# Kernel optimization log

Hardware: AMD Instinct MI355X
Metric: run time of the kernel (lower is better)

## Reference

```python
import jax, jax.numpy as jnp
import numpy as np

BATCH = 64
SEQ = 128
EMBED_DIM = 512
H = 1024
VOCAB = 32000


def setup_inputs() -> dict:
    key = jax.random.key(0)
    ks = jax.random.split(key, 10)
    prob = jax.random.randint(ks[0], (BATCH, SEQ), 0, VOCAB, dtype=jnp.int64)
    ans = jax.random.randint(ks[1], (BATCH,), 0, 10, dtype=jnp.int64)
    # nn.Embedding default init: N(0,1)
    embed_table = jax.random.normal(ks[2], (VOCAB, EMBED_DIM), jnp.float32)
    # nn.LSTMCell default init: U(-1/sqrt(h), 1/sqrt(h)), gates packed [i,f,g,o]
    k = 1.0 / np.sqrt(H).astype(np.float32)
    w_ih = jax.random.uniform(ks[3], (4 * H, EMBED_DIM), jnp.float32, -k, k)
    w_hh = jax.random.uniform(ks[4], (4 * H, H), jnp.float32, -k, k)
    b_ih = jax.random.uniform(ks[5], (4 * H,), jnp.float32, -k, k)
    b_hh = jax.random.uniform(ks[6], (4 * H,), jnp.float32, -k, k)
    # ansProj: Linear(h, 1)
    w_ans = jax.random.uniform(ks[7], (1, H), jnp.float32, -k, k)
    b_ans = jax.random.uniform(ks[7], (1,), jnp.float32, -k, k)
    # forward draws 0.01*randn initial states; pass them in for determinism
    h0 = 0.01 * jax.random.normal(ks[8], (BATCH, H), jnp.float32)
    c0 = 0.01 * jax.random.normal(ks[9], (BATCH, H), jnp.float32)
    return dict(prob=prob, ans=ans, embed_table=embed_table, w_ih=w_ih,
                w_hh=w_hh, b_ih=b_ih, b_hh=b_hh, w_ans=w_ans, b_ans=b_ans,
                h0=h0, c0=c0)


def reference(prob, ans, embed_table, w_ih, w_hh, b_ih, b_hh, w_ans, b_ans, h0, c0):
    del ans  # unpacked but unused in the original forward
    batch, seq = prob.shape
    num_unary = (seq - 2) // 2
    emb = embed_table[prob]                        # [B, S, E]
    xs = jnp.swapaxes(emb[:, :seq - 1], 0, 1)      # [T=S-1, B, E]

    def step(carry, x):
        h, c = carry
        gates = x @ w_ih.T + b_ih + h @ w_hh.T + b_hh   # [B, 4H]
        i, f, g, o = jnp.split(gates, 4, axis=-1)
        i = jax.nn.sigmoid(i)
        f = jax.nn.sigmoid(f)
        g = jnp.tanh(g)
        o = jax.nn.sigmoid(o)
        c = f * c + i * g
        h = o * jnp.tanh(c)
        return (h, c), h

    _, hs = jax.lax.scan(step, (h0, c0), xs)       # [T, B, H]
    preds = hs @ w_ans.T + b_ans                   # [T, B, 1]
    sel = preds[num_unary + 2:, :, 0]              # kept steps i > numUnary+1
    return sel.T                                   # [B, T-numUnary-2]
```

## Files before the change

kernel.cpp:

```cpp
#include <hip/hip_runtime.h>
#include <math.h>

#define BATCH   64
#define SEQLEN  128
#define EMBED   512
#define HID     1024
#define NSTEP   127
#define OUT0    65
#define NOUT    62

typedef unsigned short ushort_t;
typedef __attribute__((ext_vector_type(8))) __bf16 bf16x8;
typedef __attribute__((ext_vector_type(4))) float  f32x4;

__device__ __forceinline__ float sigmoidf_(float x) { return 1.f / (1.f + expf(-x)); }

__device__ __forceinline__ ushort_t f2bf(float f) {
    unsigned u = __builtin_bit_cast(unsigned, f);
    unsigned r = (u + 0x7FFFu + ((u >> 16) & 1u)) >> 16;
    return (ushort_t)r;
}
__device__ __forceinline__ float bf2f(ushort_t s) {
    unsigned u = ((unsigned)s) << 16;
    return __builtin_bit_cast(float, u);
}


__global__ __launch_bounds__(256) void init_mfma(
    const float* __restrict__ h0, const float* __restrict__ c0,
    float* __restrict__ cT, ushort_t* __restrict__ hf_hi, ushort_t* __restrict__ hf_lo)
{
    int id = blockIdx.x * 256 + threadIdx.x;
    int u = id >> 6, b = id & 63;
    cT[id] = c0[b * HID + u];
    float h = h0[b * HID + u];
    ushort_t hs = f2bf(h);
    ushort_t ls = f2bf(h - bf2f(hs));
    size_t idx = (((size_t)(u >> 5)) * 4 + (b >> 4)) * 512
               + ((((u & 31) >> 3) * 16) + (b & 15)) * 8 + (u & 7);
    hf_hi[idx] = hs;
    hf_lo[idx] = ls;
}

__global__ __launch_bounds__(256) void embed_frag(
    const int* __restrict__ prob, const float* __restrict__ embed,
    ushort_t* __restrict__ xf_hi, ushort_t* __restrict__ xf_lo)
{
    int t = blockIdx.x;
    for (int e = threadIdx.x; e < 4096; e += 256) {
        int b  = e >> 6;
        int kb = e & 63;
        int k  = kb * 8;
        int tok = prob[b * SEQLEN + t];
        const float* row = embed + (size_t)tok * EMBED + k;
        float4 f0 = *(const float4*)(row);
        float4 f1 = *(const float4*)(row + 4);
        float fv[8] = { f0.x, f0.y, f0.z, f0.w, f1.x, f1.y, f1.z, f1.w };
        bf16x8 hv, lv;
        #pragma unroll
        for (int i = 0; i < 8; ++i) {
            ushort_t hs = f2bf(fv[i]);
            ushort_t ls = f2bf(fv[i] - bf2f(hs));
            hv[i] = __builtin_bit_cast(__bf16, hs);
            lv[i] = __builtin_bit_cast(__bf16, ls);
        }
        size_t idx = (((size_t)t * 16 + (kb >> 2)) * 4 + (b >> 4)) * 512
                   + (((kb & 3) * 16) + (b & 15)) * 8;
        *(bf16x8*)(xf_hi + idx) = hv;
        *(bf16x8*)(xf_lo + idx) = lv;
    }
}

__global__ __launch_bounds__(1024) void lstm_mfma(
    const ushort_t* __restrict__ xf_hi, const ushort_t* __restrict__ xf_lo,
    ushort_t* __restrict__ hf_hi, ushort_t* __restrict__ hf_lo,
    const float* __restrict__ cT,
    const float* __restrict__ w_ih, const float* __restrict__ w_hh,
    const float* __restrict__ b_ih, const float* __restrict__ b_hh,
    const float* __restrict__ w_ans, float* __restrict__ pout,
    int* __restrict__ bar)
{
    extern __shared__ ushort_t smem[];
    ushort_t* a_hi = smem;
    ushort_t* a_lo = smem + 48 * 512;
    float*    redA = (float*)(smem + 96 * 512);
    float*    redB = redA + 2048;

    const int tid = threadIdx.x;
    const int bid = blockIdx.x;
    const int w   = tid >> 6;
    const int wn  = w & 3;
    const int kq  = w >> 2;
    const int L   = tid & 63;
    const int n   = L & 15;
    const int q   = L >> 4;
    const int u0  = bid * 4;
    const int ug  = u0 + q;
    const int bg  = wn * 16 + n;

    int* cnt  = bar + (bid & 7) * 32;
    int* scnt = bar + 256;
    int* go   = bar + 288;

    for (int m = 0; m < 16; ++m) {
        int unit = m >> 2, gate = m & 3;
        size_t rowg = (size_t)gate * HID + u0 + unit;
        for (int k = tid; k < 1536; k += 1024) {
            float f = (k < EMBED) ? w_ih[rowg * EMBED + k]
                                  : w_hh[rowg * HID + (k - EMBED)];
            ushort_t hs = f2bf(f);
            ushort_t ls = f2bf(f - bf2f(hs));
            int off = (k >> 5) * 512 + (((k & 31) >> 3) * 16 + m) * 8 + (k & 7);
            a_hi[off] = hs;
            a_lo[off] = ls;
        }
    }

    float c = cT[ug * 64 + bg];
    float bs[4];
    #pragma unroll
    for (int j = 0; j < 4; ++j) bs[j] = b_ih[j * HID + ug] + b_hh[j * HID + ug];
    const float wansu = w_ans[ug];
    __syncthreads();

    for (int t = 0; t < NSTEP; ++t) {
        f32x4 acc = {0.f, 0.f, 0.f, 0.f};

        {
            const ushort_t* xh = xf_hi + (((size_t)t * 16 + kq * 4) * 4 + wn) * 512 + L * 8;
            const ushort_t* xl = xf_lo + (((size_t)t * 16 + kq * 4) * 4 + wn) * 512 + L * 8;
            bf16x8 bh = *(const bf16x8*)(xh);
            bf16x8 bl = *(const bf16x8*)(xl);
            #pragma unroll
            for (int ks = 0; ks < 4; ++ks) {
                bf16x8 bh1, bl1;
                if (ks < 3) {
                    bh1 = *(const bf16x8*)(xh + (size_t)(ks + 1) * 2048);
                    bl1 = *(const bf16x8*)(xl + (size_t)(ks + 1) * 2048);
                }
                bf16x8 ah = *(const bf16x8*)(a_hi + (kq * 4 + ks) * 512 + L * 8);
                bf16x8 al = *(const bf16x8*)(a_lo + (kq * 4 + ks) * 512 + L * 8);
                acc = __builtin_amdgcn_mfma_f32_16x16x32_bf16(ah, bh, acc, 0, 0, 0);
                acc = __builtin_amdgcn_mfma_f32_16x16x32_bf16(al, bh, acc, 0, 0, 0);
                acc = __builtin_amdgcn_mfma_f32_16x16x32_bf16(ah, bl, acc, 0, 0, 0);
                bh = bh1; bl = bl1;
            }
        }

        if (t > 0) {
            while (__hip_atomic_load(go, __ATOMIC_RELAXED,
                                     __HIP_MEMORY_SCOPE_AGENT) < t)
                __builtin_amdgcn_s_sleep(1);
            __builtin_amdgcn_fence(__ATOMIC_ACQUIRE, "workgroup");
        }

        {
            const ushort_t* hh = hf_hi + (((size_t)t * 32 + kq * 8) * 4 + wn) * 512 + L * 8;
            const ushort_t* hl = hf_lo + (((size_t)t * 32 + kq * 8) * 4 + wn) * 512 + L * 8;
            bf16x8 bh = *(const bf16x8*)(hh);
            bf16x8 bl = *(const bf16x8*)(hl);
            #pragma unroll
            for (int ks = 0; ks < 8; ++ks) {
                bf16x8 bh1, bl1;
                if (ks < 7) {
                    bh1 = *(const bf16x8*)(hh + (size_t)(ks + 1) * 2048);
                    bl1 = *(const bf16x8*)(hl + (size_t)(ks + 1) * 2048);
                }
                bf16x8 ah = *(const bf16x8*)(a_hi + (16 + kq * 8 + ks) * 512 + L * 8);
                bf16x8 al = *(const bf16x8*)(a_lo + (16 + kq * 8 + ks) * 512 + L * 8);
                acc = __builtin_amdgcn_mfma_f32_16x16x32_bf16(ah, bh, acc, 0, 0, 0);
                acc = __builtin_amdgcn_mfma_f32_16x16x32_bf16(al, bh, acc, 0, 0, 0);
                acc = __builtin_amdgcn_mfma_f32_16x16x32_bf16(ah, bl, acc, 0, 0, 0);
                bh = bh1; bl = bl1;
            }
        }

        if (kq >= 2)
            *(f32x4*)(redA + ((w - 8) * 64 + L) * 4) = acc;
        __syncthreads();
        if (kq < 2) {
            f32x4 r = *(const f32x4*)(redA + (w * 64 + L) * 4);
            acc += r;
        }
        if (kq == 1)
            *(f32x4*)(redB + ((w - 4) * 64 + L) * 4) = acc;
        __syncthreads();

        if (kq == 0) {
            f32x4 r = *(const f32x4*)(redB + (w * 64 + L) * 4);
            acc += r;

            float ig = sigmoidf_(acc[0] + bs[0]);
            float fg = sigmoidf_(acc[1] + bs[1]);
            float gg = tanhf    (acc[2] + bs[2]);
            float og = sigmoidf_(acc[3] + bs[3]);
            c = fg * c + ig * gg;
            float h_new = og * tanhf(c);

            float p = h_new * wansu;
            p += __shfl_xor(p, 16, 64);
            p += __shfl_xor(p, 32, 64);
            if (t >= OUT0 && q == 0)
                pout[((size_t)(t - OUT0) * 256 + bid) * 64 + bg] = p;

            ushort_t hs = f2bf(h_new);
            ushort_t ls = f2bf(h_new - bf2f(hs));
            int kr = ug & 31, hks = ug >> 5;
            size_t idx = (((size_t)(t + 1) * 32 + hks) * 4 + wn) * 512
                       + (((kr >> 3) * 16) + n) * 8 + (kr & 7);
            __hip_atomic_store(&hf_hi[idx], hs, __ATOMIC_RELAXED,
                               __HIP_MEMORY_SCOPE_AGENT);
            __hip_atomic_store(&hf_lo[idx], ls, __ATOMIC_RELAXED,
                               __HIP_MEMORY_SCOPE_AGENT);
        }

        if (t == NSTEP - 1) break;

        __syncthreads();
        if (tid == 0) {
            int r = __hip_atomic_fetch_add(cnt, 1, __ATOMIC_RELAXED,
                                           __HIP_MEMORY_SCOPE_AGENT);
            if (r == 32 * (t + 1) - 1) {
                int s2 = __hip_atomic_fetch_add(scnt, 1, __ATOMIC_RELAXED,
                                                __HIP_MEMORY_SCOPE_AGENT);
                if (s2 == 8 * (t + 1) - 1)
                    __hip_atomic_store(go, t + 1, __ATOMIC_RELAXED,
                                       __HIP_MEMORY_SCOPE_AGENT);
            }
        }
    }
}

__global__ __launch_bounds__(256) void finalize_mfma(
    const float* __restrict__ pout, const float* __restrict__ b_ans,
    float* __restrict__ out)
{
    __shared__ float r[256];
    int col = blockIdx.x;
    int tid = threadIdx.x;
    int b = tid & 63, qq = tid >> 6;
    float s = 0.f;
    for (int i = qq; i < 256; i += 4)
        s += pout[((size_t)col * 256 + i) * 64 + b];
    r[tid] = s;
    __syncthreads();
    if (tid < 64)
        out[tid * NOUT + col] = r[tid] + r[64 + tid] + r[128 + tid] + r[192 + tid]
                              + b_ans[0];
}

#define NBLK    512
#define NTHR    512
#define REDA_OFF 12288
#define REDB_OFF 14336
#define REDC_OFF 15360
#define C_OFF    15872
#define HEAD_OFF 16000
#define LDS_FLOATS 16128

__global__ __launch_bounds__(256) void init_state(
    const float* __restrict__ h0, const float* __restrict__ c0,
    float* __restrict__ hT, float* __restrict__ cT)
{
    int id = blockIdx.x * 256 + threadIdx.x;
    int u = id >> 6, b = id & 63;
    hT[id] = h0[b * HID + u];
    cT[id] = c0[b * HID + u];
}

__global__ __launch_bounds__(256) void embed_transpose(
    const int* __restrict__ prob, const float* __restrict__ embed,
    float* __restrict__ xT)
{
    __shared__ float xe[64 * 132];
    int t = blockIdx.x;
    int tid = threadIdx.x;
    for (int kt = 0; kt < 4; ++kt) {
        #pragma unroll
        for (int i = 0; i < 8; ++i) {
            int id = tid + i * 256;
            int b  = id >> 5;
            int k4 = id & 31;
            int tok = prob[b * SEQLEN + t];
            float4 v = *(const float4*)(embed + (size_t)tok * EMBED + kt * 128 + k4 * 4);
            *(float4*)(&xe[b * 132 + k4 * 4]) = v;
        }
        __syncthreads();
        #pragma unroll
        for (int i = 0; i < 8; ++i) {
            int id = tid + i * 256;
            int kl = id >> 4;
            int b4 = id & 15;
            float4 v;
            v.x = xe[(b4 * 4 + 0) * 132 + kl];
            v.y = xe[(b4 * 4 + 1) * 132 + kl];
            v.z = xe[(b4 * 4 + 2) * 132 + kl];
            v.w = xe[(b4 * 4 + 3) * 132 + kl];
            *(float4*)(&xT[((size_t)t * EMBED + kt * 128 + kl) * 64 + b4 * 4]) = v;
        }
        __syncthreads();
    }
}

__global__ __launch_bounds__(NTHR, 4) void lstm_persist_hist(
    const float* __restrict__ xT, float* __restrict__ h_hist,
    const float* __restrict__ cT,
    const float* __restrict__ w_ih, const float* __restrict__ w_hh,
    const float* __restrict__ b_ih, const float* __restrict__ b_hh,
    const float* __restrict__ w_ans, float* __restrict__ pout,
    int* __restrict__ bar)
{
    __shared__ float lds[LDS_FLOATS];
    const int tid = threadIdx.x;
    const int bid = blockIdx.x;
    const int b   = tid & 63;
    const int ksl = __builtin_amdgcn_readfirstlane(tid >> 6);
    const int u0  = bid * 2;

    int* sliceCnt = bar + (bid >> 6) * 32;
    int* mySlice  = bar + 256 + (bid >> 6) * 32;
    int* waitGo   = bar + 256 + ksl * 32;

    for (int idx = tid; idx < 12288; idx += NTHR) {
        int r  = idx / 1536;
        int k  = idx - r * 1536;
        int u2 = r & 1, gate = r >> 1;
        int row = gate * HID + u0 + u2;
        float v = (k < EMBED) ? w_ih[(size_t)row * EMBED + k]
                              : w_hh[(size_t)row * HID + (k - EMBED)];
        lds[(u2 * 1536 + k) * 4 + gate] = v;
    }
    if (tid < 128) lds[C_OFF + tid] = cT[u0 * 64 + tid];

    float bias[2][4], wans[2];
    #pragma unroll
    for (int uu = 0; uu < 2; ++uu) {
        #pragma unroll
        for (int j = 0; j < 4; ++j) {
            int rj = j * HID + u0 + uu;
            bias[uu][j] = b_ih[rj] + b_hh[rj];
        }
        wans[uu] = w_ans[u0 + uu];
    }
    __syncthreads();

    for (int t = 0; t < NSTEP; ++t) {
        const float* xt = xT + (size_t)t * EMBED * 64;
        const float* ht = h_hist + (size_t)t * HID * 64;
        float* hn_buf   = h_hist + (size_t)(t + 1) * HID * 64;

        float acc[2][4];
        #pragma unroll
        for (int uu = 0; uu < 2; ++uu)
            #pragma unroll
            for (int j = 0; j < 4; ++j) acc[uu][j] = 0.f;

        const int kx0 = ksl * 64;
        #pragma unroll 4
        for (int g = 0; g < 16; ++g) {
            const int k = kx0 + g * 4;
            float xv[4];
            #pragma unroll
            for (int i = 0; i < 4; ++i) xv[i] = xt[(size_t)(k + i) * 64 + b];
            #pragma unroll
            for (int i = 0; i < 4; ++i) {
                float4 wa = *(const float4*)&lds[(0 * 1536 + k + i) * 4];
                float4 wb = *(const float4*)&lds[(1 * 1536 + k + i) * 4];
                acc[0][0] = fmaf(wa.x, xv[i], acc[0][0]);
                acc[0][1] = fmaf(wa.y, xv[i], acc[0][1]);
                acc[0][2] = fmaf(wa.z, xv[i], acc[0][2]);
                acc[0][3] = fmaf(wa.w, xv[i], acc[0][3]);
                acc[1][0] = fmaf(wb.x, xv[i], acc[1][0]);
                acc[1][1] = fmaf(wb.y, xv[i], acc[1][1]);
                acc[1][2] = fmaf(wb.z, xv[i], acc[1][2]);
                acc[1][3] = fmaf(wb.w, xv[i], acc[1][3]);
            }
        }

        if (t > 0) {
            while (__hip_atomic_load(waitGo, __ATOMIC_RELAXED,
                                     __HIP_MEMORY_SCOPE_AGENT) < t)
                __builtin_amdgcn_s_sleep(4);
            __builtin_amdgcn_fence(__ATOMIC_ACQUIRE, "workgroup");
        }

        const int kh0 = ksl * 128;
        #pragma unroll 4
        for (int g = 0; g < 32; ++g) {
            const int kh = kh0 + g * 4;
            float hv[4];
            #pragma unroll
            for (int i = 0; i < 4; ++i)
                hv[i] = ht[(size_t)(kh + i) * 64 + b];
            #pragma unroll
            for (int i = 0; i < 4; ++i) {
                const int kw = EMBED + kh + i;
                float4 wa = *(const float4*)&lds[(0 * 1536 + kw) * 4];
                float4 wb = *(const float4*)&lds[(1 * 1536 + kw) * 4];
                acc[0][0] = fmaf(wa.x, hv[i], acc[0][0]);
                acc[0][1] = fmaf(wa.y, hv[i], acc[0][1]);
                acc[0][2] = fmaf(wa.z, hv[i], acc[0][2]);
                acc[0][3] = fmaf(wa.w, hv[i], acc[0][3]);
                acc[1][0] = fmaf(wb.x, hv[i], acc[1][0]);
                acc[1][1] = fmaf(wb.y, hv[i], acc[1][1]);
                acc[1][2] = fmaf(wb.z, hv[i], acc[1][2]);
                acc[1][3] = fmaf(wb.w, hv[i], acc[1][3]);
            }
        }

        if (ksl >= 4) {
            #pragma unroll
            for (int uu = 0; uu < 2; ++uu)
                #pragma unroll
                for (int j = 0; j < 4; ++j)
                    lds[REDA_OFF + (((ksl - 4) * 8) + uu * 4 + j) * 64 + b] = acc[uu][j];
        }
        __syncthreads();
        if (ksl < 4) {
            #pragma unroll
            for (int uu = 0; uu < 2; ++uu)
                #pragma unroll
                for (int j = 0; j < 4; ++j)
                    acc[uu][j] += lds[REDA_OFF + ((ksl * 8) + uu * 4 + j) * 64 + b];
        }
        if (ksl == 2 || ksl == 3) {
            #pragma unroll
            for (int uu = 0; uu < 2; ++uu)
                #pragma unroll
                for (int j = 0; j < 4; ++j)
                    lds[REDB_OFF + (((ksl - 2) * 8) + uu * 4 + j) * 64 + b] = acc[uu][j];
        }
        __syncthreads();
        if (ksl < 2) {
            #pragma unroll
            for (int uu = 0; uu < 2; ++uu)
                #pragma unroll
                for (int j = 0; j < 4; ++j)
                    acc[uu][j] += lds[REDB_OFF + ((ksl * 8) + uu * 4 + j) * 64 + b];
        }
        if (ksl == 0) {
            #pragma unroll
            for (int j = 0; j < 4; ++j)
                lds[REDC_OFF + j * 64 + b] = acc[1][j];
        }
        if (ksl == 1) {
            #pragma unroll
            for (int j = 0; j < 4; ++j)
                lds[REDC_OFF + (4 + j) * 64 + b] = acc[0][j];
        }
        __syncthreads();
        if (ksl < 2) {
            const int uu = ksl;
            float s[4];
            if (ksl == 0) {
                #pragma unroll
                for (int j = 0; j < 4; ++j)
                    s[j] = acc[0][j] + lds[REDC_OFF + (4 + j) * 64 + b];
            } else {
                #pragma unroll
                for (int j = 0; j < 4; ++j)
                    s[j] = acc[1][j] + lds[REDC_OFF + j * 64 + b];
            }
            float i_g = sigmoidf_(s[0] + bias[uu][0]);
            float f_g = sigmoidf_(s[1] + bias[uu][1]);
            float g_g = tanhf   (s[2] + bias[uu][2]);
            float o_g = sigmoidf_(s[3] + bias[uu][3]);
            float c_old = lds[C_OFF + uu * 64 + b];
            float c_new = f_g * c_old + i_g * g_g;
            float h_new = o_g * tanhf(c_new);
            lds[C_OFF + uu * 64 + b] = c_new;
            __hip_atomic_store(&hn_buf[(u0 + uu) * 64 + b], h_new,
                               __ATOMIC_RELAXED, __HIP_MEMORY_SCOPE_AGENT);
            lds[HEAD_OFF + uu * 64 + b] = h_new * wans[uu];
        }

        __syncthreads();
        if (t >= OUT0 && tid < 64) {
            pout[((size_t)(t - OUT0) * NBLK + bid) * 64 + tid] =
                lds[HEAD_OFF + tid] + lds[HEAD_OFF + 64 + tid];
        }
        if (t == NSTEP - 1) break;
        if (tid == 0) {
            int r = __hip_atomic_fetch_add(sliceCnt, 1, __ATOMIC_RELAXED,
                                           __HIP_MEMORY_SCOPE_AGENT);
            if (r == 64 * (t + 1) - 1)
                __hip_atomic_store(mySlice, t + 1, __ATOMIC_RELAXED,
                                   __HIP_MEMORY_SCOPE_AGENT);
        }
    }
}

__global__ __launch_bounds__(256) void finalize_persist(
    const float* __restrict__ pout, const float* __restrict__ b_ans,
    float* __restrict__ out)
{
    __shared__ float r[256];
    int col = blockIdx.x;
    int tid = threadIdx.x;
    int b = tid & 63, qq = tid >> 6;
    float s = 0.f;
    for (int i = qq; i < NBLK; i += 4)
        s += pout[((size_t)col * NBLK + i) * 64 + b];
    r[tid] = s;
    __syncthreads();
    if (tid < 64)
        out[tid * NOUT + col] = r[tid] + r[64 + tid] + r[128 + tid] + r[192 + tid]
                              + b_ans[0];
}

extern "C" void kernel_launch(void* const* d_in, const int* in_sizes, int n_in,
                              void* d_out, int out_size, void* d_ws, size_t ws_size,
                              hipStream_t stream)
{
    const int*   prob  = (const int*)  d_in[0];
    const float* embed = (const float*)d_in[2];
    const float* w_ih  = (const float*)d_in[3];
    const float* w_hh  = (const float*)d_in[4];
    const float* b_ih  = (const float*)d_in[5];
    const float* b_hh  = (const float*)d_in[6];
    const float* w_ans = (const float*)d_in[7];
    const float* b_ans = (const float*)d_in[8];
    const float* h0    = (const float*)d_in[9];
    const float* c0    = (const float*)d_in[10];

    char* W = (char*)d_ws;
    float*    cT_m  = (float*)   (W);
    float*    poutm = (float*)   (W + 262144);
    ushort_t* xf_hi = (ushort_t*)(W + 4325376);
    ushort_t* xf_lo = (ushort_t*)(W + 12648448);
    ushort_t* hf_hi = (ushort_t*)(W + 20971520);
    ushort_t* hf_lo = (ushort_t*)(W + 37748736);
    int*      bar_m = (int*)     (W + 54525952);

    const int DYN_LDS = 96 * 1024 + 12288;

    hipError_t err = hipFuncSetAttribute(
        (const void*)lstm_mfma,
        hipFuncAttributeMaxDynamicSharedMemorySize, DYN_LDS);

    if (err == hipSuccess) {
        hipMemsetAsync(bar_m, 0, 2048, stream);
        init_mfma<<<256, 256, 0, stream>>>(h0, c0, cT_m, hf_hi, hf_lo);
        embed_frag<<<NSTEP, 256, 0, stream>>>(prob, embed, xf_hi, xf_lo);

        void* args[] = {
            (void*)&xf_hi, (void*)&xf_lo, (void*)&hf_hi, (void*)&hf_lo,
            (void*)&cT_m, (void*)&w_ih, (void*)&w_hh, (void*)&b_ih,
            (void*)&b_hh, (void*)&w_ans, (void*)&poutm, (void*)&bar_m
        };
        err = hipLaunchCooperativeKernel((const void*)lstm_mfma,
                                         dim3(256), dim3(1024),
                                         args, DYN_LDS, stream);
        if (err == hipSuccess) {
            finalize_mfma<<<NOUT, 256, 0, stream>>>(poutm, b_ans, (float*)d_out);
            return;
        }
    }

    float* ws     = (float*)d_ws;
    float* cT     = ws;
    float* pout   = ws + 65536;
    float* xT     = ws + 2097152;
    float* h_hist = ws + 6258688;
    int*   bar    = (int*)(ws + 14647296);

    hipMemsetAsync(bar, 0, 2048, stream);
    init_state<<<256, 256, 0, stream>>>(h0, c0, h_hist, cT);
    embed_transpose<<<NSTEP, 256, 0, stream>>>(prob, embed, xT);

    void* args9[] = {
        (void*)&xT, (void*)&h_hist, (void*)&cT,
        (void*)&w_ih, (void*)&w_hh, (void*)&b_ih, (void*)&b_hh,
        (void*)&w_ans, (void*)&pout, (void*)&bar
    };
    hipLaunchCooperativeKernel((const void*)lstm_persist_hist,
                               dim3(NBLK), dim3(NTHR), args9, 0, stream);
    finalize_persist<<<NOUT, 256, 0, stream>>>(pout, b_ans, (float*)d_out);
}
```

Measured before the change: 902.5 us.

## Replace global barrier with per-wave arrival counters and split embed kernel

Replaces the hierarchical grid barrier (block counter, super counter, go flag) with per-wave arrival counters grouped by hidden-slice. Each wave polls only the eight counters covering the k-range of h it consumes. Each wave signals as soon as its own h stores have drained, and there is no __syncthreads. This removes the serial chain of atomics and the block-wide sync on each of the 127 recurrent steps, at the cost of more polling traffic and subtler memory-ordering assumptions. The embedding conversion kernel is also split across four times as many blocks for more parallelism.

After: 977.7 us. 1.08x slower.

```diff
diff --git a/kernel.cpp b/kernel.cpp
--- a/kernel.cpp
+++ b/kernel.cpp
@@ -46,8 +46,12 @@
     const int* __restrict__ prob, const float* __restrict__ embed,
     ushort_t* __restrict__ xf_hi, ushort_t* __restrict__ xf_lo)
 {
-    int t = blockIdx.x;
-    for (int e = threadIdx.x; e < 4096; e += 256) {
+    int t  = blockIdx.x >> 2;
+    int qd = blockIdx.x & 3;
+    if (t >= NSTEP) return;
+    #pragma unroll
+    for (int i = 0; i < 4; ++i) {
+        int e = qd * 1024 + threadIdx.x + i * 256;
         int b  = e >> 6;
         int kb = e & 63;
         int k  = kb * 8;
@@ -58,11 +62,11 @@
         float fv[8] = { f0.x, f0.y, f0.z, f0.w, f1.x, f1.y, f1.z, f1.w };
         bf16x8 hv, lv;
         #pragma unroll
-        for (int i = 0; i < 8; ++i) {
-            ushort_t hs = f2bf(fv[i]);
-            ushort_t ls = f2bf(fv[i] - bf2f(hs));
-            hv[i] = __builtin_bit_cast(__bf16, hs);
-            lv[i] = __builtin_bit_cast(__bf16, ls);
+        for (int j = 0; j < 8; ++j) {
+            ushort_t hs = f2bf(fv[j]);
+            ushort_t ls = f2bf(fv[j] - bf2f(hs));
+            hv[j] = __builtin_bit_cast(__bf16, hs);
+            lv[j] = __builtin_bit_cast(__bf16, ls);
         }
         size_t idx = (((size_t)t * 16 + (kb >> 2)) * 4 + (b >> 4)) * 512
                    + (((kb & 3) * 16) + (b & 15)) * 8;
@@ -98,9 +102,8 @@
     const int ug  = u0 + q;
     const int bg  = wn * 16 + n;
 
-    int* cnt  = bar + (bid & 7) * 32;
-    int* scnt = bar + 256;
-    int* go   = bar + 288;
+    int* myArrive  = bar + (bid >> 6) * 256 + (bid & 7) * 32;
+    int* pollBase  = bar + kq * 256;
 
     for (int m = 0; m < 16; ++m) {
         int unit = m >> 2, gate = m & 3;
@@ -148,9 +151,13 @@
         }
 
         if (t > 0) {
-            while (__hip_atomic_load(go, __ATOMIC_RELAXED,
-                                     __HIP_MEMORY_SCOPE_AGENT) < t)
+            const int target = 32 * t;
+            for (;;) {
+                int v = __hip_atomic_load(pollBase + (L & 7) * 32,
+                                          __ATOMIC_RELAXED, __HIP_MEMORY_SCOPE_AGENT);
+                if (__ballot(v >= target) == ~0ULL) break;
                 __builtin_amdgcn_s_sleep(1);
+            }
             __builtin_amdgcn_fence(__ATOMIC_ACQUIRE, "workgroup");
         }
 
@@ -212,20 +219,12 @@
                                __HIP_MEMORY_SCOPE_AGENT);
             __hip_atomic_store(&hf_lo[idx], ls, __ATOMIC_RELAXED,
                                __HIP_MEMORY_SCOPE_AGENT);
-        }
-
-        if (t == NSTEP - 1) break;
-
-        __syncthreads();
-        if (tid == 0) {
-            int r = __hip_atomic_fetch_add(cnt, 1, __ATOMIC_RELAXED,
+
+            if (t < NSTEP - 1) {
+                asm volatile("s_waitcnt vmcnt(0)" ::: "memory");
+                if (L == 0)
+                    __hip_atomic_fetch_add(myArrive, 1, __ATOMIC_RELAXED,
                                            __HIP_MEMORY_SCOPE_AGENT);
-            if (r == 32 * (t + 1) - 1) {
-                int s2 = __hip_atomic_fetch_add(scnt, 1, __ATOMIC_RELAXED,
-                                                __HIP_MEMORY_SCOPE_AGENT);
-                if (s2 == 8 * (t + 1) - 1)
-                    __hip_atomic_store(go, t + 1, __ATOMIC_RELAXED,
-                                       __HIP_MEMORY_SCOPE_AGENT);
             }
         }
     }
@@ -539,9 +538,9 @@
         hipFuncAttributeMaxDynamicSharedMemorySize, DYN_LDS);
 
     if (err == hipSuccess) {
-        hipMemsetAsync(bar_m, 0, 2048, stream);
+        hipMemsetAsync(bar_m, 0, 4096, stream);
         init_mfma<<<256, 256, 0, stream>>>(h0, c0, cT_m, hf_hi, hf_lo);
-        embed_frag<<<NSTEP, 256, 0, stream>>>(prob, embed, xf_hi, xf_lo);
+        embed_frag<<<NSTEP * 4, 256, 0, stream>>>(prob, embed, xf_hi, xf_lo);
 
         void* args[] = {
             (void*)&xf_hi, (void*)&xf_lo, (void*)&hf_hi, (void*)&hf_lo,
```
